# Optimization experiments

Measured on AMD Instinct MI355X. Metric: run time of the kernel, lower is better.

The kernel has to match this reference:

```python
import jax, jax.numpy as jnp
import numpy as np

N_NODES = 100000
N_EDGES = 1600000
B = 16
NMAX = 4096
IN_DIM = 32
H1 = 64      # capacity C
H2 = 128     # 2C
LAT = 64
DEC_H = 128  # 2C
DEC_IN = LAT + 2
FUEL = 5


def _ln(x, g, b):
    m = x.mean(-1, keepdims=True)
    v = x.var(-1, keepdims=True)
    return (x - m) / jnp.sqrt(v + 1e-5) * g + b


def _mlp2(x, wi, bi, g, be, wo, bo):
    # DeepMLP with num_layers=2: in_lin -> LayerNorm -> ReLU -> out_lin
    h = jax.nn.relu(_ln(x @ wi + bi, g, be))
    return h @ wo + bo


def setup_inputs() -> dict:
    key = jax.random.key(0)
    ks = jax.random.split(key, 48)
    d = {}
    d['x'] = jax.random.normal(ks[0], (N_NODES, IN_DIM), jnp.float32)
    d['edge_index'] = jax.random.randint(ks[1], (2, N_EDGES), 0, N_NODES)
    d['batch'] = jnp.sort(jax.random.randint(ks[2], (N_NODES,), 0, B))

    def w(k, shape):
        return (jax.random.normal(k, shape, jnp.float32) * 0.02)

    conv_shapes = {'w1m': (IN_DIM, H1), 'w2m': (H1, H2), 'w3m': (H2, LAT),
                   'w1l': (IN_DIM, H1), 'w2l': (H1, H2), 'w3l': (H2, LAT)}
    i = 3
    for nm, sh in conv_shapes.items():
        d[nm] = w(ks[i], sh); i += 1
        d['b' + nm[1:]] = jnp.zeros((sh[1],), jnp.float32)
    # node_mlp (DeepMLP dec_in->dec_h->dec_h)
    d['nm_wi'] = w(ks[i], (DEC_IN, DEC_H)); i += 1
    d['nm_bi'] = jnp.zeros((DEC_H,), jnp.float32)
    d['nm_g'] = jnp.ones((DEC_H,), jnp.float32)
    d['nm_be'] = jnp.zeros((DEC_H,), jnp.float32)
    d['nm_wo'] = w(ks[i], (DEC_H, DEC_H)); i += 1
    d['nm_bo'] = jnp.zeros((DEC_H,), jnp.float32)
    # heads
    d['ex_w'] = w(ks[i], (DEC_H, 1)); i += 1
    d['ex_b'] = jnp.zeros((1,), jnp.float32)
    d['fu_w'] = w(ks[i], (DEC_H, FUEL)); i += 1
    d['fu_b'] = jnp.zeros((FUEL,), jnp.float32)
    d['al_w'] = w(ks[i], (DEC_H, 1)); i += 1
    d['al_b'] = jnp.zeros((1,), jnp.float32)
    d['sl_w'] = w(ks[i], (DEC_H, 1)); i += 1
    d['sl_b'] = jnp.zeros((1,), jnp.float32)
    # edge_mlp (DeepMLP dec_in->dec_h->8)
    d['em_wi'] = w(ks[i], (DEC_IN, DEC_H)); i += 1
    d['em_bi'] = jnp.zeros((DEC_H,), jnp.float32)
    d['em_g'] = jnp.ones((DEC_H,), jnp.float32)
    d['em_be'] = jnp.zeros((DEC_H,), jnp.float32)
    d['em_wo'] = w(ks[i], (DEC_H, 8)); i += 1
    d['em_bo'] = jnp.zeros((8,), jnp.float32)
    d['pos_all'] = jax.random.normal(ks[i], (NMAX, 2), jnp.float32)
    return d


def reference(x, edge_index, batch,
              w1m, b1m, w2m, b2m, w3m, b3m,
              w1l, b1l, w2l, b2l, w3l, b3l,
              nm_wi, nm_bi, nm_g, nm_be, nm_wo, nm_bo,
              ex_w, ex_b, fu_w, fu_b, al_w, al_b, sl_w, sl_b,
              em_wi, em_bi, em_g, em_be, em_wo, em_bo,
              pos_all):
    # ---- GCN encoder with self-loops and symmetric normalization (PyG GCNConv) ----
    loops = jnp.arange(N_NODES)
    src = jnp.concatenate([edge_index[0], loops])
    dst = jnp.concatenate([edge_index[1], loops])
    deg = jax.ops.segment_sum(jnp.ones(src.shape, jnp.float32), dst, N_NODES)
    dinv = jax.lax.rsqrt(deg)  # deg >= 1 because of self-loops
    norm = (dinv[src] * dinv[dst])[:, None]

    def conv(h, wt, bt):
        hw = h @ wt                                   # [N, F_out]
        return jax.ops.segment_sum(norm * hw[src], dst, N_NODES) + bt

    mu = jax.nn.relu(conv(x, w1m, b1m))
    mu = jax.nn.relu(conv(mu, w2m, b2m))
    mu = jax.nn.relu(conv(mu, w3m, b3m))
    lg = jax.nn.relu(conv(x, w1l, b1l))
    lg = jax.nn.relu(conv(lg, w2l, b2l))
    lg = jax.nn.relu(conv(lg, w3l, b3l))

    cnt = jnp.maximum(jax.ops.segment_sum(jnp.ones((N_NODES,), jnp.float32), batch, B), 1.0)[:, None]
    mu_g = jax.ops.segment_sum(mu, batch, B) / cnt    # global_mean_pool [B, LAT]
    lg_g = jax.ops.segment_sum(lg, batch, B) / cnt

    z = mu_g  # eval-mode latent_sample returns mu

    # ---- decoder ----
    Z = jnp.broadcast_to(z[:, None, :], (B, NMAX, LAT))
    pos = jnp.broadcast_to(pos_all[None], (B, NMAX, 2))
    Zp = jnp.concatenate([Z, pos], -1).reshape(B * NMAX, DEC_IN)
    h = _mlp2(Zp, nm_wi, nm_bi, nm_g, nm_be, nm_wo, nm_bo)
    nodes = (h @ ex_w + ex_b).reshape(B, NMAX, 1)
    fuel = (h @ fu_w + fu_b).reshape(B, NMAX, FUEL)
    alt = (h @ al_w + al_b).reshape(B, NMAX, 1)
    slope = (h @ sl_w + sl_b).reshape(B, NMAX, 1)
    edges = _mlp2(Zp, em_wi, em_bi, em_g, em_be, em_wo, em_bo).reshape(B, NMAX, 8)
    return (nodes, edges, fuel, alt, slope, mu_g, lg_g)
```

## Files before the change

### kernel.cpp

```cpp
#include <hip/hip_runtime.h>
#include <hip/hip_bf16.h>

#define N_NODES 100000
#define N_EDGESC 1600000
#define BATCH_B 16
#define NMAXC 4096
#define LATC 64
#define NBINS 391
#define NSB 256
#define EPB ((N_EDGESC + NSB - 1) / NSB)
#define BIN_PAD 768

#define OUT_NODES 0
#define OUT_EDGES 65536
#define OUT_FUEL  589824
#define OUT_ALT   917504
#define OUT_SLOPE 983040
#define OUT_MU    1048576
#define OUT_LG    1049600

typedef float f32x2 __attribute__((ext_vector_type(2)));
typedef float f32x4 __attribute__((ext_vector_type(4)));
typedef short bf16x8 __attribute__((ext_vector_type(8)));
union U4B { uint4 u; bf16x8 b; };

__device__ __forceinline__ unsigned short f2bf(float f) {
    unsigned int u = __float_as_uint(f);
    return (unsigned short)((u + 0x7FFFu + ((u >> 16) & 1u)) >> 16);
}
__device__ __forceinline__ float bf2f(unsigned short h) {
    return __uint_as_float(((unsigned int)h) << 16);
}
__device__ __forceinline__ void f8acc(unsigned int u, float& a0, float& a1, float& a2, float& a3) {
    f32x2 lo = __builtin_amdgcn_cvt_pk_f32_fp8(u, false);
    f32x2 hi = __builtin_amdgcn_cvt_pk_f32_fp8(u, true);
    a0 += lo[0]; a1 += lo[1]; a2 += hi[0]; a3 += hi[1];
}

__global__ void batch_count(const int* __restrict__ batch, int* __restrict__ bcnt, int n) {
    int b = threadIdx.x;
    if (b >= BATCH_B) return;
    int lo = 0, hi = n;
    while (lo < hi) { int mid = (lo + hi) >> 1; if (batch[mid] < b) lo = mid + 1; else hi = mid; }
    int start = lo;
    lo = 0; hi = n;
    while (lo < hi) { int mid = (lo + hi) >> 1; if (batch[mid] <= b) lo = mid + 1; else hi = mid; }
    bcnt[b] = lo - start;
}

__global__ __launch_bounds__(1024) void histA(const int* __restrict__ dst, int* __restrict__ hist) {
    __shared__ int h[NBINS];
    int b = blockIdx.x, t = threadIdx.x;
    for (int i = t; i < NBINS; i += 1024) h[i] = 0;
    __syncthreads();
    int e0 = b * EPB, e1 = min(e0 + EPB, N_EDGESC);
    for (int i = e0 + t; i < e1; i += 1024)
        atomicAdd(&h[dst[i] >> 8], 1);
    __syncthreads();
    for (int i = t; i < NBINS; i += 1024) hist[i * NSB + b] = h[i];
}

__global__ void scanB(int* __restrict__ hist, int* __restrict__ total) {
    __shared__ int sh[NSB];
    int j = blockIdx.x, t = threadIdx.x;
    int v = hist[j * NSB + t];
    sh[t] = v; __syncthreads();
    for (int off = 1; off < NSB; off <<= 1) {
        int u = (t >= off) ? sh[t - off] : 0; __syncthreads();
        sh[t] += u; __syncthreads();
    }
    hist[j * NSB + t] = sh[t] - v;
    if (t == NSB - 1) total[j] = sh[t];
}

__global__ void scanC(const int* __restrict__ total, int* __restrict__ base) {
    __shared__ int sh[512];
    int t = threadIdx.x;
    int v = (t < NBINS) ? total[t] : 0;
    sh[t] = v; __syncthreads();
    for (int off = 1; off < 512; off <<= 1) {
        int u = (t >= off) ? sh[t - off] : 0; __syncthreads();
        sh[t] += u; __syncthreads();
    }
    if (t < NBINS) base[t] = sh[t] - v;
    if (t == NBINS - 1) base[NBINS] = sh[t];
}

__global__ __launch_bounds__(1024) void scatterD(const int* __restrict__ src, const int* __restrict__ dst,
                                                 const int* __restrict__ hist, const int* __restrict__ base,
                                                 unsigned int* __restrict__ sorted) {
    __shared__ int w0[NBINS];
    __shared__ int lc[NBINS];
    int b = blockIdx.x, t = threadIdx.x;
    for (int i = t; i < NBINS; i += 1024) {
        w0[i] = base[i] + hist[i * NSB + b];
        lc[i] = 0;
    }
    __syncthreads();
    int e0 = b * EPB, e1 = min(e0 + EPB, N_EDGESC);
    for (int i = e0 + t; i < e1; i += 1024) {
        int d = dst[i], s = src[i];
        int j = d >> 8;
        int r = atomicAdd(&lc[j], 1);
        sorted[w0[j] + r] = ((unsigned int)s << 8) | (d & 255);
    }
}

__global__ void csr_compact(const unsigned int* __restrict__ sorted, const int* __restrict__ base,
                            int* __restrict__ adj, int* __restrict__ offs,
                            int* __restrict__ cnt, float* __restrict__ dinv, int N) {
    __shared__ int lc[256];
    __shared__ int cur[256];
    __shared__ int so4[256];
    int j = blockIdx.x, t = threadIdx.x;
    lc[t] = 0; cur[t] = 0;
    __syncthreads();
    int e0 = base[j], e1 = base[j + 1];
    for (int i = e0 + t; i < e1; i += 256)
        atomicAdd(&lc[sorted[i] & 255], 1);
    __syncthreads();
    int c4 = (lc[t] + 3) & ~3;
    so4[t] = c4;
    __syncthreads();
    for (int off = 1; off < 256; off <<= 1) {
        int u = (t >= off) ? so4[t - off] : 0; __syncthreads();
        so4[t] += u; __syncthreads();
    }
    int mybase = base[j] + j * BIN_PAD + so4[t] - c4;
    __syncthreads();
    so4[t] = mybase;
    __syncthreads();
    for (int i = e0 + t; i < e1; i += 256) {
        unsigned int pk = sorted[i];
        int d = pk & 255;
        int r = atomicAdd(&cur[d], 1);
        adj[so4[d] + r] = (int)(pk >> 8);
    }
    int n = j * 256 + t;
    if (n < N) {
        cnt[n] = lc[t];
        offs[n] = so4[t];
        dinv[n] = rsqrtf((float)(lc[t] + 1));
    }
}

__global__ void prescale_x(const float* __restrict__ x, const float* __restrict__ dinv,
                           unsigned int* __restrict__ xs8, int total4) {
    int i4 = blockIdx.x * 256 + threadIdx.x;
    if (i4 < total4) {
        float4 v = *(const float4*)&x[i4 * 4];
        float ds = dinv[i4 >> 3] * 64.f;
        unsigned int r = 0;
        r = __builtin_amdgcn_cvt_pk_fp8_f32(v.x * ds, v.y * ds, r, false);
        r = __builtin_amdgcn_cvt_pk_fp8_f32(v.z * ds, v.w * ds, r, true);
        xs8[i4] = r;
    }
}

__global__ void agg_s32(const unsigned int* __restrict__ xs8, const int* __restrict__ cnt,
                        const int* __restrict__ offs, const int* __restrict__ adj,
                        const float* __restrict__ dinv, float* __restrict__ out, int N) {
    int t = threadIdx.x;
    int sub = t >> 3, f = t & 7;
    int n = blockIdx.x * 32 + sub;
    if (n >= N) return;
    float s0 = 0.f, s1 = 0.f, s2 = 0.f, s3 = 0.f;
    f8acc(xs8[(size_t)n * 8 + f], s0, s1, s2, s3);
    int e = offs[n];
    int e1 = e + cnt[n];
    for (; e + 8 <= e1; e += 8) {
        int4 ia = *(const int4*)&adj[e];
        int4 ib = *(const int4*)&adj[e + 4];
        unsigned int u0 = xs8[(size_t)ia.x * 8 + f];
        unsigned int u1 = xs8[(size_t)ia.y * 8 + f];
        unsigned int u2 = xs8[(size_t)ia.z * 8 + f];
        unsigned int u3 = xs8[(size_t)ia.w * 8 + f];
        unsigned int u4 = xs8[(size_t)ib.x * 8 + f];
        unsigned int u5 = xs8[(size_t)ib.y * 8 + f];
        unsigned int u6 = xs8[(size_t)ib.z * 8 + f];
        unsigned int u7 = xs8[(size_t)ib.w * 8 + f];
        f8acc(u0, s0, s1, s2, s3); f8acc(u1, s0, s1, s2, s3);
        f8acc(u2, s0, s1, s2, s3); f8acc(u3, s0, s1, s2, s3);
        f8acc(u4, s0, s1, s2, s3); f8acc(u5, s0, s1, s2, s3);
        f8acc(u6, s0, s1, s2, s3); f8acc(u7, s0, s1, s2, s3);
    }
    if (e + 4 <= e1) {
        int4 ia = *(const int4*)&adj[e];
        unsigned int u0 = xs8[(size_t)ia.x * 8 + f];
// ... 38 lines not shown
        f8acc(u4, s0, s1, s2, s3); f8acc(u5, s0, s1, s2, s3);
        f8acc(u6, s0, s1, s2, s3); f8acc(u7, s0, s1, s2, s3);
    }
    if (e + 4 <= e1) {
        int4 ia = *(const int4*)&adj[e];
        unsigned int u0 = tbl[(size_t)ia.x * 32 + f];
        unsigned int u1 = tbl[(size_t)ia.y * 32 + f];
        unsigned int u2 = tbl[(size_t)ia.z * 32 + f];
        unsigned int u3 = tbl[(size_t)ia.w * 32 + f];
        f8acc(u0, s0, s1, s2, s3); f8acc(u1, s0, s1, s2, s3);
        f8acc(u2, s0, s1, s2, s3); f8acc(u3, s0, s1, s2, s3);
        e += 4;
    }
    for (; e < e1; e++) f8acc(tbl[(size_t)adj[e] * 32 + f], s0, s1, s2, s3);
    float d = dinv[n] * (1.f / 32.f);
    float v0 = s0 * d, v1 = s1 * d, v2 = s2 * d, v3 = s3 * d;
    if (BIASRELU) {
        float4 bv = *(const float4*)&bias[4 * f];
        v0 = fmaxf(v0 + bv.x, 0.f); v1 = fmaxf(v1 + bv.y, 0.f);
        v2 = fmaxf(v2 + bv.z, 0.f); v3 = fmaxf(v3 + bv.w, 0.f);
    }
    if (OUT8) {
        unsigned int r = 0;
        r = __builtin_amdgcn_cvt_pk_fp8_f32(v0 * 32.f, v1 * 32.f, r, false);
        r = __builtin_amdgcn_cvt_pk_fp8_f32(v2 * 32.f, v3 * 32.f, r, true);
        ((unsigned int*)outv)[(size_t)n * 32 + f] = r;
    } else {
        ushort4 u;
        u.x = f2bf(v0); u.y = f2bf(v1); u.z = f2bf(v2); u.w = f2bf(v3);
        *(ushort4*)&((unsigned short*)outv)[(size_t)n * 128 + 4 * f] = u;
    }
}

template <int K, int F>
__global__ void wprep(const float* __restrict__ Wa, const float* __restrict__ Wb,
                      unsigned int* __restrict__ wfrag) {
    constexpr int S = K / 32, C = F / 16;
    int lane = threadIdx.x;
    int bc = blockIdx.x;
    int c = bc % C;
    int s = (bc / C) % S;
    int y = bc / (C * S);
    const float* W = (y == 0) ? Wa : Wb;
    int col = c * 16 + (lane & 15);
    int k0 = s * 32 + (lane >> 4) * 8;
    unsigned int q[4];
#pragma unroll
    for (int jj = 0; jj < 4; jj++) {
        float lo = W[(size_t)(k0 + 2 * jj) * F + col];
        float hi = W[(size_t)(k0 + 2 * jj + 1) * F + col];
        q[jj] = (unsigned int)f2bf(lo) | ((unsigned int)f2bf(hi) << 16);
    }
    *(uint4*)&wfrag[((size_t)bc * 64 + lane) * 4] = make_uint4(q[0], q[1], q[2], q[3]);
}

template <int K, int F, int IN_STRIDE, int IN_OFF_Y, int OUT_STRIDE, int OUT_OFF_Y,
          bool BIASRELU, bool SCALE, int INMODE, int OUTMODE>
__global__ __launch_bounds__(256) void mfma_conv(
    const void* __restrict__ inv, const unsigned int* __restrict__ wfrag,
    const float* __restrict__ biasa, const float* __restrict__ biasb,
    const float* __restrict__ dinv, void* __restrict__ outv, int N) {
    constexpr int S = K / 32, C = F / 16;
    constexpr int FP = F + 4;
    __shared__ unsigned short buf[4][16][FP];
    int t = threadIdx.x, lane = t & 63, wave = t >> 6;
    int y = blockIdx.y;
    int n0 = blockIdx.x * 64 + wave * 16;
    const float* bias = (y == 0) ? biasa : biasb;
    const unsigned int* wf = wfrag + (size_t)y * S * C * 64 * 4;

    f32x4 acc[C];
#pragma unroll
    for (int c = 0; c < C; c++) acc[c] = (f32x4)(0.f);

    int arow = n0 + (lane & 15);
    bool aok = arow < N;
#pragma unroll
    for (int s = 0; s < S; s++) {
        U4B af; af.u = make_uint4(0u, 0u, 0u, 0u);
        if (aok) {
            if constexpr (INMODE == 2) {
                uint2 u = *(const uint2*)((const unsigned char*)inv +
                            (size_t)arow * IN_STRIDE + y * IN_OFF_Y + s * 32 + (lane >> 4) * 8);
                f32x2 p0 = __builtin_amdgcn_cvt_pk_f32_fp8(u.x, false);
                f32x2 p1 = __builtin_amdgcn_cvt_pk_f32_fp8(u.x, true);
                f32x2 p2 = __builtin_amdgcn_cvt_pk_f32_fp8(u.y, false);
                f32x2 p3 = __builtin_amdgcn_cvt_pk_f32_fp8(u.y, true);
                af.u.x = (unsigned int)f2bf(p0[0]) | ((unsigned int)f2bf(p0[1]) << 16);
                af.u.y = (unsigned int)f2bf(p1[0]) | ((unsigned int)f2bf(p1[1]) << 16);
                af.u.z = (unsigned int)f2bf(p2[0]) | ((unsigned int)f2bf(p2[1]) << 16);
                af.u.w = (unsigned int)f2bf(p3[0]) | ((unsigned int)f2bf(p3[1]) << 16);
            } else if constexpr (INMODE == 1) {
                af.u = *(const uint4*)((const unsigned short*)inv +
                            (size_t)arow * IN_STRIDE + y * IN_OFF_Y + s * 32 + (lane >> 4) * 8);
            } else {
                const float* ap = (const float*)inv + (size_t)arow * IN_STRIDE + y * IN_OFF_Y
                                  + s * 32 + (lane >> 4) * 8;
                float4 v0 = *(const float4*)ap;
                float4 v1 = *(const float4*)(ap + 4);
                af.u.x = (unsigned int)f2bf(v0.x) | ((unsigned int)f2bf(v0.y) << 16);
                af.u.y = (unsigned int)f2bf(v0.z) | ((unsigned int)f2bf(v0.w) << 16);
                af.u.z = (unsigned int)f2bf(v1.x) | ((unsigned int)f2bf(v1.y) << 16);
                af.u.w = (unsigned int)f2bf(v1.z) | ((unsigned int)f2bf(v1.w) << 16);
            }
        }
#pragma unroll
        for (int c = 0; c < C; c++) {
            U4B wb;
            wb.u = *(const uint4*)&wf[((size_t)(s * C + c) * 64 + lane) * 4];
            acc[c] = __builtin_amdgcn_mfma_f32_16x16x32_bf16(af.b, wb.b, acc[c], 0, 0, 0);
        }
    }

    constexpr float ISC = (INMODE == 2) ? (1.f / 32.f) : 1.f;
#pragma unroll
    for (int c = 0; c < C; c++) {
        int col = c * 16 + (lane & 15);
        float bv = BIASRELU ? bias[col] : 0.f;
#pragma unroll
        for (int r = 0; r < 4; r++) {
            int row = (lane >> 4) * 4 + r;
            int n = n0 + row;
            float v = acc[c][r] * ISC;
            if (BIASRELU) v = fmaxf(v + bv, 0.f);
            if (SCALE) v *= dinv[min(n, N - 1)];
            buf[wave][row][col] = f2bf(v);
        }
    }
    __syncthreads();

    constexpr int CPR = F / 8;
    for (int i = t; i < 64 * CPR; i += 256) {
        int row = i / CPR;
        int f0 = (i % CPR) * 8;
        int n = blockIdx.x * 64 + row;
        if (n >= N) continue;
        const unsigned short* bp = &buf[row >> 4][row & 15][f0];
        uint2 a = *(const uint2*)bp;
        uint2 b = *(const uint2*)(bp + 4);
        size_t off = (size_t)n * OUT_STRIDE + y * OUT_OFF_Y + f0;
        if constexpr (OUTMODE == 2) {
            float e0 = __uint_as_float(a.x << 16), e1 = __uint_as_float(a.x & 0xFFFF0000u);
            float e2 = __uint_as_float(a.y << 16), e3 = __uint_as_float(a.y & 0xFFFF0000u);
            float e4 = __uint_as_float(b.x << 16), e5 = __uint_as_float(b.x & 0xFFFF0000u);
            float e6 = __uint_as_float(b.y << 16), e7 = __uint_as_float(b.y & 0xFFFF0000u);
            unsigned int r0 = 0, r1 = 0;
            r0 = __builtin_amdgcn_cvt_pk_fp8_f32(e0 * 32.f, e1 * 32.f, r0, false);
            r0 = __builtin_amdgcn_cvt_pk_fp8_f32(e2 * 32.f, e3 * 32.f, r0, true);
            r1 = __builtin_amdgcn_cvt_pk_fp8_f32(e4 * 32.f, e5 * 32.f, r1, false);
            r1 = __builtin_amdgcn_cvt_pk_fp8_f32(e6 * 32.f, e7 * 32.f, r1, true);
            *(uint2*)((unsigned char*)outv + off) = make_uint2(r0, r1);
        } else {
            *(uint4*)((unsigned short*)outv + off) = make_uint4(a.x, a.y, b.x, b.y);
        }
    }
}

__global__ void prep_cat(const float* __restrict__ w1m, const float* __restrict__ w1l,
                         const float* __restrict__ b1m, const float* __restrict__ b1l,
                         const float* __restrict__ b3m, const float* __restrict__ b3l,
                         float* __restrict__ wcat1, float* __restrict__ bcat1,
                         float* __restrict__ bcat3) {
    int i = blockIdx.x * 256 + threadIdx.x;
    if (i < 32 * 128) {
        int k = i >> 7, f = i & 127;
        wcat1[i] = (f < 64) ? w1m[k * 64 + f] : w1l[k * 64 + f - 64];
    } else if (i < 32 * 128 + 128) {
        int f = i - 32 * 128;
        bcat1[f] = (f < 64) ? b1m[f] : b1l[f - 64];
    } else if (i < 32 * 128 + 256) {
        int f = i - 32 * 128 - 128;
        bcat3[f] = (f < 64) ? b3m[f] : b3l[f - 64];
    }
}

__global__ void prep_dec(const float* __restrict__ nm_wo, const float* __restrict__ nm_bo,
                         const float* __restrict__ ex_w, const float* __restrict__ ex_b,
                         const float* __restrict__ fu_w, const float* __restrict__ fu_b,
                         const float* __restrict__ al_w, const float* __restrict__ al_b,
                         const float* __restrict__ sl_w, const float* __restrict__ sl_b,
                         const float* __restrict__ em_wo,
                         float* __restrict__ wtn, float* __restrict__ bcn,
                         float* __restrict__ wte) {
    int idx = blockIdx.x * 256 + threadIdx.x;
    if (idx < 1024) {
        int j = idx >> 7, k = idx & 127;
        float s = 0.f;
        for (int m = 0; m < 128; m++) {
            float w = (j == 0) ? ex_w[m] : (j <= 5) ? fu_w[m * 5 + (j - 1)]
                     : (j == 6) ? al_w[m] : sl_w[m];
            s += nm_wo[k * 128 + m] * w;
        }
        wtn[j * 128 + k] = s;
    } else if (idx < 2048) {
        int i2 = idx - 1024;
        int j = i2 >> 7, k = i2 & 127;
        wte[j * 128 + k] = em_wo[k * 8 + j];
    } else if (idx < 2056) {
        int j = idx - 2048;
        float s = (j == 0) ? ex_b[0] : (j <= 5) ? fu_b[j - 1] : (j == 6) ? al_b[0] : sl_b[0];
        for (int m = 0; m < 128; m++) {
            float w = (j == 0) ? ex_w[m] : (j <= 5) ? fu_w[m * 5 + (j - 1)]
                     : (j == 6) ? al_w[m] : sl_w[m];
            s += nm_bo[m] * w;
        }
        bcn[j] = s;
    }
}

#define POOL_CHUNK 128
__global__ void pool128(const unsigned int* __restrict__ h, const int* __restrict__ batch,
                        float* __restrict__ sums, int n) {
    int f = threadIdx.x;
    int s0 = blockIdx.x * POOL_CHUNK;
    if (s0 >= n) return;
    int s1 = min(s0 + POOL_CHUNK, n);
    int cur = batch[s0];
    float a0 = 0.f, a1 = 0.f;
    for (int i = s0; i < s1; i++) {
        int b = batch[i];
        if (b != cur) {
            atomicAdd(&sums[cur * 128 + 2 * f], a0);
            atomicAdd(&sums[cur * 128 + 2 * f + 1], a1);
            a0 = a1 = 0.f; cur = b;
        }
        unsigned int u = h[(size_t)i * 64 + f];
        a0 += __uint_as_float(u << 16);
        a1 += __uint_as_float(u & 0xFFFF0000u);
    }
    atomicAdd(&sums[cur * 128 + 2 * f], a0);
    atomicAdd(&sums[cur * 128 + 2 * f + 1], a1);
}

__global__ void finalize_pool(const float* __restrict__ sums, const int* __restrict__ bcnt,
                              float* __restrict__ out, float* __restrict__ zbuf) {
    int i = blockIdx.x * 1024 + threadIdx.x;
    int b = i >> 7, f = i & 127;
    float c = fmaxf((float)bcnt[b], 1.f);
    float v = sums[i] / c;
    if (f < 64) { out[OUT_MU + b * 64 + f] = v; zbuf[b * 64 + f] = v; }
    else out[OUT_LG + b * 64 + (f - 64)] = v;
}

__global__ void zwi_kernel(const float* __restrict__ z,
                           const float* __restrict__ nm_wi, const float* __restrict__ nm_bi,
                           const float* __restrict__ em_wi, const float* __restrict__ em_bi,
                           float* __restrict__ zwi_nm, float* __restrict__ zwi_em) {
    int b = blockIdx.x, t = threadIdx.x;
    float an = nm_bi[t], ae = em_bi[t];
    for (int k = 0; k < 64; k++) {
        float zv = z[b * 64 + k];
        an += zv * nm_wi[k * 128 + t];
        ae += zv * em_wi[k * 128 + t];
    }
    zwi_nm[b * 128 + t] = an;
    zwi_em[b * 128 + t] = ae;
}

#define D3_ROWS 32

__global__ __launch_bounds__(256) void decoder3(
    const float* __restrict__ zwi_nm, const float* __restrict__ zwi_em,
    const float* __restrict__ nm_wi, const float* __restrict__ em_wi,
    const float* __restrict__ nm_g, const float* __restrict__ nm_be,
    const float* __restrict__ em_g, const float* __restrict__ em_be,
    const float* __restrict__ wtn, const float* __restrict__ bcn,
    const float* __restrict__ wte, const float* __restrict__ em_bo,
    const float* __restrict__ pos_all,
    float* __restrict__ out) {
    __shared__ float sn[D3_ROWS][132];
    __shared__ float se[D3_ROWS][132];
    __shared__ float Wn[8][132];
    __shared__ float We[8][132];
    int t = threadIdx.x;
    int lane = t & 63, wave = t >> 6;
    int rowBase = blockIdx.x * D3_ROWS;
    int b = rowBase >> 12;
    int row0 = rowBase + wave * 8;

    for (int i = t; i < 1024; i += 256) {
        Wn[i >> 7][i & 127] = wtn[i];
        We[i >> 7][i & 127] = wte[i];
    }

// ... 62 lines not shown
    const float* x    = (const float*)d_in[0];
    const int* edge   = (const int*)d_in[1];
    const int* batch  = (const int*)d_in[2];
    const float* w1m = (const float*)d_in[3];  const float* b1m = (const float*)d_in[4];
    const float* w2m = (const float*)d_in[5];  const float* b2m = (const float*)d_in[6];
    const float* w3m = (const float*)d_in[7];  const float* b3m = (const float*)d_in[8];
    const float* w1l = (const float*)d_in[9];  const float* b1l = (const float*)d_in[10];
    const float* w2l = (const float*)d_in[11]; const float* b2l = (const float*)d_in[12];
    const float* w3l = (const float*)d_in[13]; const float* b3l = (const float*)d_in[14];
    const float* nm_wi = (const float*)d_in[15]; const float* nm_bi = (const float*)d_in[16];
    const float* nm_g  = (const float*)d_in[17]; const float* nm_be = (const float*)d_in[18];
    const float* nm_wo = (const float*)d_in[19]; const float* nm_bo = (const float*)d_in[20];
    const float* ex_w = (const float*)d_in[21]; const float* ex_b = (const float*)d_in[22];
    const float* fu_w = (const float*)d_in[23]; const float* fu_b = (const float*)d_in[24];
    const float* al_w = (const float*)d_in[25]; const float* al_b = (const float*)d_in[26];
    const float* sl_w = (const float*)d_in[27]; const float* sl_b = (const float*)d_in[28];
    const float* em_wi = (const float*)d_in[29]; const float* em_bi = (const float*)d_in[30];
    const float* em_g  = (const float*)d_in[31]; const float* em_be = (const float*)d_in[32];
    const float* em_wo = (const float*)d_in[33]; const float* em_bo = (const float*)d_in[34];
    const float* pos_all = (const float*)d_in[35];
    float* out = (float*)d_out;

    char* p = (char*)d_ws;
    auto alloc = [&](size_t bytes) -> void* {
        void* r = (void*)p;
        p += ((bytes + 255) / 256) * 256;
        return r;
    };
    int* cnt      = (int*)alloc((size_t)N_NODES * 4);
    int* offs     = (int*)alloc((size_t)N_NODES * 4);
    float* dinv   = (float*)alloc((size_t)N_NODES * 4);
    int* bcnt     = (int*)alloc(BATCH_B * 4);
    float* sums   = (float*)alloc(BATCH_B * 128 * 4);
    float* zbuf   = (float*)alloc(BATCH_B * LATC * 4);
    float* zwi_nm = (float*)alloc(BATCH_B * 128 * 4);
    float* zwi_em = (float*)alloc(BATCH_B * 128 * 4);
    float* wcat1  = (float*)alloc(32 * 128 * 4);
    float* bcat1  = (float*)alloc(128 * 4);
    float* bcat3  = (float*)alloc(128 * 4);
    float* wtn    = (float*)alloc(8 * 128 * 4);
    float* bcn    = (float*)alloc(8 * 4);
    float* wte    = (float*)alloc(8 * 128 * 4);
    unsigned int* wf1 = (unsigned int*)alloc((size_t)1 * 1 * 8 * 64 * 4 * 4);
    unsigned int* wf2 = (unsigned int*)alloc((size_t)2 * 2 * 8 * 64 * 4 * 4);
    unsigned int* wf3 = (unsigned int*)alloc((size_t)2 * 4 * 4 * 64 * 4 * 4);
    int* hist     = (int*)alloc((size_t)NBINS * NSB * 4);
    int* total    = (int*)alloc((size_t)NBINS * 4);
    int* base     = (int*)alloc((size_t)(NBINS + 1) * 4);
    unsigned int* sorted = (unsigned int*)alloc((size_t)N_EDGESC * 4);
    int* adj      = (int*)alloc((size_t)(N_EDGESC + NBINS * BIN_PAD + 256) * 4);
    unsigned int* xs8 = (unsigned int*)alloc((size_t)N_NODES * 8 * 4);
    float* agg0   = (float*)alloc((size_t)N_NODES * 32 * 4);
    unsigned int* hA8 = (unsigned int*)alloc((size_t)N_NODES * 32 * 4);
    unsigned int* hB8 = (unsigned int*)alloc((size_t)N_NODES * 32 * 4);
    unsigned short* h256 = (unsigned short*)alloc((size_t)N_NODES * 256 * 2);
    unsigned short* final128 = (unsigned short*)alloc((size_t)N_NODES * 128 * 2);
    unsigned int* hD8 = hA8;

    const int* srcp = edge;
    const int* dstp = edge + N_EDGESC;

    hipMemsetAsync(sums, 0, (size_t)BATCH_B * 128 * 4, stream);

    histA<<<NSB, 1024, 0, stream>>>(dstp, hist);
    scanB<<<NBINS, NSB, 0, stream>>>(hist, total);
    scanC<<<1, 512, 0, stream>>>(total, base);
    scatterD<<<NSB, 1024, 0, stream>>>(srcp, dstp, hist, base, sorted);
    csr_compact<<<NBINS, 256, 0, stream>>>(sorted, base, adj, offs, cnt, dinv, N_NODES);

    batch_count<<<1, 64, 0, stream>>>(batch, bcnt, N_NODES);
    prep_cat<<<17, 256, 0, stream>>>(w1m, w1l, b1m, b1l, b3m, b3l, wcat1, bcat1, bcat3);
    prep_dec<<<9, 256, 0, stream>>>(nm_wo, nm_bo, ex_w, ex_b, fu_w, fu_b, al_w, al_b,
                                    sl_w, sl_b, em_wo, wtn, bcn, wte);
    wprep<32, 128><<<1 * 1 * 8, 64, 0, stream>>>(wcat1, wcat1, wf1);
    wprep<64, 128><<<2 * 2 * 8, 64, 0, stream>>>(w2m, w2l, wf2);
    wprep<128, 64><<<2 * 4 * 4, 64, 0, stream>>>(w3m, w3l, wf3);
    prescale_x<<<(N_NODES * 8 + 255) / 256, 256, 0, stream>>>(x, dinv, xs8, N_NODES * 8);

    agg_s32<<<(N_NODES + 31) / 32, 256, 0, stream>>>(xs8, cnt, offs, adj, dinv, agg0, N_NODES);

    const int GB = (N_NODES + 63) / 64;

    mfma_conv<32, 128, 32, 0, 128, 0, true, true, 0, 2>
        <<<dim3(GB, 1), 256, 0, stream>>>(agg0, wf1, bcat1, bcat1, dinv, hA8, N_NODES);

    agg128<false, true><<<(N_NODES + 7) / 8, 256, 0, stream>>>(
        hA8, cnt, offs, adj, dinv, nullptr, hB8, N_NODES);

    mfma_conv<64, 128, 128, 64, 256, 128, true, false, 2, 1>
        <<<dim3(GB, 2), 256, 0, stream>>>(hB8, wf2, b2m, b2l, dinv, h256, N_NODES);

    mfma_conv<128, 64, 256, 128, 128, 64, false, true, 1, 2>
        <<<dim3(GB, 2), 256, 0, stream>>>(h256, wf3, nullptr, nullptr, dinv, hD8, N_NODES);

    agg128<true, false><<<(N_NODES + 7) / 8, 256, 0, stream>>>(
        hD8, cnt, offs, adj, dinv, bcat3, final128, N_NODES);

    pool128<<<(N_NODES + POOL_CHUNK - 1) / POOL_CHUNK, 64, 0, stream>>>(
        (const unsigned int*)final128, batch, sums, N_NODES);
    finalize_pool<<<2, 1024, 0, stream>>>(sums, bcnt, out, zbuf);

    zwi_kernel<<<BATCH_B, 128, 0, stream>>>(zbuf, nm_wi, nm_bi, em_wi, em_bi, zwi_nm, zwi_em);

    decoder3<<<BATCH_B * NMAXC / D3_ROWS, 256, 0, stream>>>(
        zwi_nm, zwi_em, nm_wi, em_wi, nm_g, nm_be, em_g, em_be,
        wtn, bcn, wte, em_bo, pos_all, out);
}
```

Baseline: 297.2 us.

## Fuse prep kernels, fold x prescale into CSR compaction, fuse conv layers 2 and 3

Merges batch counting, bias concatenation, decoder weight folding and all MFMA weight-fragment preparation into one mega_prep launch. Folds the fp8 prescale of x into csr_compact, fuses the layer-2 and layer-3 dense transforms into one conv23 kernel that keeps the 128-wide hidden tile in shared memory instead of writing h256 to global, and merges pool finalization with the z·W_in kernel. The aim is to cut launch count and the round trip of the 100k x 256 bf16 intermediate, in exchange for more shared memory and register use per block in the fused conv.

Result: faster. 265.9 us (-10.5%).

```diff
diff --git a/kernel.cpp b/kernel.cpp
--- a/kernel.cpp
+++ b/kernel.cpp
@@ -36,16 +36,11 @@
     f32x2 hi = __builtin_amdgcn_cvt_pk_f32_fp8(u, true);
     a0 += lo[0]; a1 += lo[1]; a2 += hi[0]; a3 += hi[1];
 }
-
-__global__ void batch_count(const int* __restrict__ batch, int* __restrict__ bcnt, int n) {
-    int b = threadIdx.x;
-    if (b >= BATCH_B) return;
-    int lo = 0, hi = n;
-    while (lo < hi) { int mid = (lo + hi) >> 1; if (batch[mid] < b) lo = mid + 1; else hi = mid; }
-    int start = lo;
-    lo = 0; hi = n;
-    while (lo < hi) { int mid = (lo + hi) >> 1; if (batch[mid] <= b) lo = mid + 1; else hi = mid; }
-    bcnt[b] = lo - start;
+__device__ __forceinline__ void f8_to_bf2(unsigned int u, unsigned int& q0, unsigned int& q1) {
+    f32x2 lo = __builtin_amdgcn_cvt_pk_f32_fp8(u, false);
+    f32x2 hi = __builtin_amdgcn_cvt_pk_f32_fp8(u, true);
+    q0 = (unsigned int)f2bf(lo[0]) | ((unsigned int)f2bf(lo[1]) << 16);
+    q1 = (unsigned int)f2bf(hi[0]) | ((unsigned int)f2bf(hi[1]) << 16);
 }
 
 __global__ __launch_bounds__(1024) void histA(const int* __restrict__ dst, int* __restrict__ hist) {
@@ -107,8 +102,10 @@
 }
 
 __global__ void csr_compact(const unsigned int* __restrict__ sorted, const int* __restrict__ base,
+                            const float* __restrict__ x,
                             int* __restrict__ adj, int* __restrict__ offs,
-                            int* __restrict__ cnt, float* __restrict__ dinv, int N) {
+                            int* __restrict__ cnt, float* __restrict__ dinv,
+                            unsigned int* __restrict__ xs8, int N) {
     __shared__ int lc[256];
     __shared__ int cur[256];
     __shared__ int so4[256];
@@ -138,22 +135,24 @@
     }
     int n = j * 256 + t;
     if (n < N) {
-        cnt[n] = lc[t];
+        int c = lc[t];
+        cnt[n] = c;
         offs[n] = so4[t];
-        dinv[n] = rsqrtf((float)(lc[t] + 1));
-    }
-}
-
-__global__ void prescale_x(const float* __restrict__ x, const float* __restrict__ dinv,
-                           unsigned int* __restrict__ xs8, int total4) {
-    int i4 = blockIdx.x * 256 + threadIdx.x;
-    if (i4 < total4) {
-        float4 v = *(const float4*)&x[i4 * 4];
-        float ds = dinv[i4 >> 3] * 64.f;
-        unsigned int r = 0;
-        r = __builtin_amdgcn_cvt_pk_fp8_f32(v.x * ds, v.y * ds, r, false);
-        r = __builtin_amdgcn_cvt_pk_fp8_f32(v.z * ds, v.w * ds, r, true);
-        xs8[i4] = r;
+        float dv = rsqrtf((float)(c + 1));
+        dinv[n] = dv;
+        float ds = dv * 64.f;
+        const float* xr = &x[(size_t)n * 32];
+        unsigned int q[8];
+#pragma unroll
+        for (int jj = 0; jj < 8; jj++) {
+            float4 v = *(const float4*)&xr[jj * 4];
+            unsigned int r8 = 0;
+            r8 = __builtin_amdgcn_cvt_pk_fp8_f32(v.x * ds, v.y * ds, r8, false);
+            r8 = __builtin_amdgcn_cvt_pk_fp8_f32(v.z * ds, v.w * ds, r8, true);
+            q[jj] = r8;
+        }
+        *(uint4*)&xs8[(size_t)n * 8] = make_uint4(q[0], q[1], q[2], q[3]);
+        *(uint4*)&xs8[(size_t)n * 8 + 4] = make_uint4(q[4], q[5], q[6], q[7]);
     }
 }
 
@@ -258,18 +257,8 @@
     }
 }
 
-template <int K, int F>
-__global__ void wprep(const float* __restrict__ Wa, const float* __restrict__ Wb,
-                      unsigned int* __restrict__ wfrag) {
-    constexpr int S = K / 32, C = F / 16;
-    int lane = threadIdx.x;
-    int bc = blockIdx.x;
-    int c = bc % C;
-    int s = (bc / C) % S;
-    int y = bc / (C * S);
-    const float* W = (y == 0) ? Wa : Wb;
-    int col = c * 16 + (lane & 15);
-    int k0 = s * 32 + (lane >> 4) * 8;
+__device__ __forceinline__ void wfrag_write(const float* W, int F, int col, int k0,
+                                            unsigned int* dst) {
     unsigned int q[4];
 #pragma unroll
     for (int jj = 0; jj < 4; jj++) {
@@ -277,23 +266,107 @@
         float hi = W[(size_t)(k0 + 2 * jj + 1) * F + col];
         q[jj] = (unsigned int)f2bf(lo) | ((unsigned int)f2bf(hi) << 16);
     }
-    *(uint4*)&wfrag[((size_t)bc * 64 + lane) * 4] = make_uint4(q[0], q[1], q[2], q[3]);
-}
-
-template <int K, int F, int IN_STRIDE, int IN_OFF_Y, int OUT_STRIDE, int OUT_OFF_Y,
-          bool BIASRELU, bool SCALE, int INMODE, int OUTMODE>
-__global__ __launch_bounds__(256) void mfma_conv(
-    const void* __restrict__ inv, const unsigned int* __restrict__ wfrag,
-    const float* __restrict__ biasa, const float* __restrict__ biasb,
-    const float* __restrict__ dinv, void* __restrict__ outv, int N) {
-    constexpr int S = K / 32, C = F / 16;
-    constexpr int FP = F + 4;
+    *(uint4*)dst = make_uint4(q[0], q[1], q[2], q[3]);
+}
+
+__global__ void mega_prep(const int* __restrict__ batch,
+                          const float* __restrict__ w1m, const float* __restrict__ w1l,
+                          const float* __restrict__ b1m, const float* __restrict__ b1l,
+                          const float* __restrict__ b3m, const float* __restrict__ b3l,
+                          const float* __restrict__ w2m, const float* __restrict__ w2l,
+                          const float* __restrict__ w3m, const float* __restrict__ w3l,
+                          const float* __restrict__ nm_wo, const float* __restrict__ nm_bo,
+                          const float* __restrict__ ex_w, const float* __restrict__ ex_b,
+                          const float* __restrict__ fu_w, const float* __restrict__ fu_b,
+                          const float* __restrict__ al_w, const float* __restrict__ al_b,
+                          const float* __restrict__ sl_w, const float* __restrict__ sl_b,
+                          const float* __restrict__ em_wo,
+                          int* __restrict__ bcnt, float* __restrict__ bcat1,
+                          float* __restrict__ bcat3, float* __restrict__ wtn,
+                          float* __restrict__ bcn, float* __restrict__ wte,
+                          unsigned int* __restrict__ wf1, unsigned int* __restrict__ wf2,
+                          unsigned int* __restrict__ wf3) {
+    int blk = blockIdx.x, t = threadIdx.x;
+    if (blk == 0) {
+        if (t < 128) bcat1[t] = (t < 64) ? b1m[t] : b1l[t - 64];
+        else { int f = t - 128; bcat3[f] = (f < 64) ? b3m[f] : b3l[f - 64]; }
+        if (t < BATCH_B) {
+            int b = t;
+            int lo = 0, hi = N_NODES;
+            while (lo < hi) { int mid = (lo + hi) >> 1; if (batch[mid] < b) lo = mid + 1; else hi = mid; }
+            int start = lo;
+            lo = 0; hi = N_NODES;
+            while (lo < hi) { int mid = (lo + hi) >> 1; if (batch[mid] <= b) lo = mid + 1; else hi = mid; }
+            bcnt[b] = lo - start;
+        }
+    } else if (blk <= 9) {
+        int idx = (blk - 1) * 256 + t;
+        if (idx < 1024) {
+            int j = idx >> 7, k = idx & 127;
+            float s = 0.f;
+            for (int m = 0; m < 128; m++) {
+                float w = (j == 0) ? ex_w[m] : (j <= 5) ? fu_w[m * 5 + (j - 1)]
+                         : (j == 6) ? al_w[m] : sl_w[m];
+                s += nm_wo[k * 128 + m] * w;
+            }
+            wtn[j * 128 + k] = s;
+        } else if (idx < 2048) {
+            int i2 = idx - 1024;
+            int j = i2 >> 7, k = i2 & 127;
+            wte[j * 128 + k] = em_wo[k * 8 + j];
+        } else if (idx < 2056) {
+            int j = idx - 2048;
+            float s = (j == 0) ? ex_b[0] : (j <= 5) ? fu_b[j - 1] : (j == 6) ? al_b[0] : sl_b[0];
+            for (int m = 0; m < 128; m++) {
+                float w = (j == 0) ? ex_w[m] : (j <= 5) ? fu_w[m * 5 + (j - 1)]
+                         : (j == 6) ? al_w[m] : sl_w[m];
+                s += nm_bo[m] * w;
+            }
+            bcn[j] = s;
+        }
+    } else if (blk <= 17) {
+        if (t < 64) {
+            int c = blk - 10;
+            int col = c * 16 + (t & 15);
+            int k0 = (t >> 4) * 8;
+            unsigned int q[4];
+#pragma unroll
+            for (int jj = 0; jj < 4; jj++) {
+                int ka = k0 + 2 * jj, kb = ka + 1;
+                float lo = (col < 64) ? w1m[ka * 64 + col] : w1l[ka * 64 + col - 64];
+                float hi = (col < 64) ? w1m[kb * 64 + col] : w1l[kb * 64 + col - 64];
+                q[jj] = (unsigned int)f2bf(lo) | ((unsigned int)f2bf(hi) << 16);
+            }
+            *(uint4*)&wf1[((size_t)c * 64 + t) * 4] = make_uint4(q[0], q[1], q[2], q[3]);
+        }
+    } else if (blk <= 49) {
+        if (t < 64) {
+            int bc = blk - 18;
+            int c = bc % 8, s = (bc / 8) % 2, y = bc / 16;
+            const float* W = y ? w2l : w2m;
+            wfrag_write(W, 128, c * 16 + (t & 15), s * 32 + (t >> 4) * 8,
+                        &wf2[((size_t)bc * 64 + t) * 4]);
+        }
+    } else {
+        if (t < 64) {
+            int bc = blk - 50;
+            int c = bc % 4, s = (bc / 4) % 4, y = bc / 16;
+            const float* W = y ? w3l : w3m;
+            wfrag_write(W, 64, c * 16 + (t & 15), s * 32 + (t >> 4) * 8,
+                        &wf3[((size_t)bc * 64 + t) * 4]);
+        }
+    }
+}
+
+__global__ __launch_bounds__(256) void mfma_conv1(
+    const float* __restrict__ inv, const unsigned int* __restrict__ wfrag,
+    const float* __restrict__ bias, const float* __restrict__ dinv,
+    unsigned int* __restrict__ outv, int N) {
+    constexpr int C = 8;
+    constexpr int FP = 132;
     __shared__ unsigned short buf[4][16][FP];
     int t = threadIdx.x, lane = t & 63, wave = t >> 6;
-    int y = blockIdx.y;
     int n0 = blockIdx.x * 64 + wave * 16;
-    const float* bias = (y == 0) ? biasa : biasb;
-    const unsigned int* wf = wfrag + (size_t)y * S * C * 64 * 4;
 
     f32x4 acc[C];
 #pragma unroll
@@ -301,136 +374,149 @@
 
     int arow = n0 + (lane & 15);
     bool aok = arow < N;
-#pragma unroll
-    for (int s = 0; s < S; s++) {
-        U4B af; af.u = make_uint4(0u, 0u, 0u, 0u);
-        if (aok) {
-            if constexpr (INMODE == 2) {
-                uint2 u = *(const uint2*)((const unsigned char*)inv +
-                            (size_t)arow * IN_STRIDE + y * IN_OFF_Y + s * 32 + (lane >> 4) * 8);
-                f32x2 p0 = __builtin_amdgcn_cvt_pk_f32_fp8(u.x, false);
-                f32x2 p1 = __builtin_amdgcn_cvt_pk_f32_fp8(u.x, true);
-                f32x2 p2 = __builtin_amdgcn_cvt_pk_f32_fp8(u.y, false);
-                f32x2 p3 = __builtin_amdgcn_cvt_pk_f32_fp8(u.y, true);
-                af.u.x = (unsigned int)f2bf(p0[0]) | ((unsigned int)f2bf(p0[1]) << 16);
-                af.u.y = (unsigned int)f2bf(p1[0]) | ((unsigned int)f2bf(p1[1]) << 16);
-                af.u.z = (unsigned int)f2bf(p2[0]) | ((unsigned int)f2bf(p2[1]) << 16);
-                af.u.w = (unsigned int)f2bf(p3[0]) | ((unsigned int)f2bf(p3[1]) << 16);
-            } else if constexpr (INMODE == 1) {
-                af.u = *(const uint4*)((const unsigned short*)inv +
-                            (size_t)arow * IN_STRIDE + y * IN_OFF_Y + s * 32 + (lane >> 4) * 8);
-            } else {
-                const float* ap = (const float*)inv + (size_t)arow * IN_STRIDE + y * IN_OFF_Y
-                                  + s * 32 + (lane >> 4) * 8;
-                float4 v0 = *(const float4*)ap;
-                float4 v1 = *(const float4*)(ap + 4);
-                af.u.x = (unsigned int)f2bf(v0.x) | ((unsigned int)f2bf(v0.y) << 16);
-                af.u.y = (unsigned int)f2bf(v0.z) | ((unsigned int)f2bf(v0.w) << 16);
-                af.u.z = (unsigned int)f2bf(v1.x) | ((unsigned int)f2bf(v1.y) << 16);
-                af.u.w = (unsigned int)f2bf(v1.z) | ((unsigned int)f2bf(v1.w) << 16);
-            }
-        }
-#pragma unroll
-        for (int c = 0; c < C; c++) {
-            U4B wb;
-            wb.u = *(const uint4*)&wf[((size_t)(s * C + c) * 64 + lane) * 4];
-            acc[c] = __builtin_amdgcn_mfma_f32_16x16x32_bf16(af.b, wb.b, acc[c], 0, 0, 0);
-        }
-    }
-
-    constexpr float ISC = (INMODE == 2) ? (1.f / 32.f) : 1.f;
+    U4B af; af.u = make_uint4(0u, 0u, 0u, 0u);
+    if (aok) {
+        const float* ap = inv + (size_t)arow * 32 + (lane >> 4) * 8;
+        float4 v0 = *(const float4*)ap;
+        float4 v1 = *(const float4*)(ap + 4);
+        af.u.x = (unsigned int)f2bf(v0.x) | ((unsigned int)f2bf(v0.y) << 16);
+        af.u.y = (unsigned int)f2bf(v0.z) | ((unsigned int)f2bf(v0.w) << 16);
+        af.u.z = (unsigned int)f2bf(v1.x) | ((unsigned int)f2bf(v1.y) << 16);
+        af.u.w = (unsigned int)f2bf(v1.z) | ((unsigned int)f2bf(v1.w) << 16);
+    }
+#pragma unroll
+    for (int c = 0; c < C; c++) {
+        U4B wb;
+        wb.u = *(const uint4*)&wfrag[((size_t)c * 64 + lane) * 4];
+        acc[c] = __builtin_amdgcn_mfma_f32_16x16x32_bf16(af.b, wb.b, acc[c], 0, 0, 0);
+    }
+
 #pragma unroll
     for (int c = 0; c < C; c++) {
         int col = c * 16 + (lane & 15);
-        float bv = BIASRELU ? bias[col] : 0.f;
+        float bv = bias[col];
 #pragma unroll
         for (int r = 0; r < 4; r++) {
             int row = (lane >> 4) * 4 + r;
             int n = n0 + row;
-            float v = acc[c][r] * ISC;
-            if (BIASRELU) v = fmaxf(v + bv, 0.f);
-            if (SCALE) v *= dinv[min(n, N - 1)];
+            float v = fmaxf(acc[c][r] + bv, 0.f) * dinv[min(n, N - 1)];
             buf[wave][row][col] = f2bf(v);
         }
     }
     __syncthreads();
 
-    constexpr int CPR = F / 8;
-    for (int i = t; i < 64 * CPR; i += 256) {
-        int row = i / CPR;
-        int f0 = (i % CPR) * 8;
+    for (int i = t; i < 64 * 16; i += 256) {
+        int row = i / 16;
+        int f0 = (i % 16) * 8;
         int n = blockIdx.x * 64 + row;
         if (n >= N) continue;
         const unsigned short* bp = &buf[row >> 4][row & 15][f0];
         uint2 a = *(const uint2*)bp;
         uint2 b = *(const uint2*)(bp + 4);
-        size_t off = (size_t)n * OUT_STRIDE + y * OUT_OFF_Y + f0;
-        if constexpr (OUTMODE == 2) {
-            float e0 = __uint_as_float(a.x << 16), e1 = __uint_as_float(a.x & 0xFFFF0000u);
-            float e2 = __uint_as_float(a.y << 16), e3 = __uint_as_float(a.y & 0xFFFF0000u);
-            float e4 = __uint_as_float(b.x << 16), e5 = __uint_as_float(b.x & 0xFFFF0000u);
-            float e6 = __uint_as_float(b.y << 16), e7 = __uint_as_float(b.y & 0xFFFF0000u);
-            unsigned int r0 = 0, r1 = 0;
-            r0 = __builtin_amdgcn_cvt_pk_fp8_f32(e0 * 32.f, e1 * 32.f, r0, false);
-            r0 = __builtin_amdgcn_cvt_pk_fp8_f32(e2 * 32.f, e3 * 32.f, r0, true);
-            r1 = __builtin_amdgcn_cvt_pk_fp8_f32(e4 * 32.f, e5 * 32.f, r1, false);
-            r1 = __builtin_amdgcn_cvt_pk_fp8_f32(e6 * 32.f, e7 * 32.f, r1, true);
-            *(uint2*)((unsigned char*)outv + off) = make_uint2(r0, r1);
-        } else {
-            *(uint4*)((unsigned short*)outv + off) = make_uint4(a.x, a.y, b.x, b.y);
-        }
-    }
-}
-
-__global__ void prep_cat(const float* __restrict__ w1m, const float* __restrict__ w1l,
-                         const float* __restrict__ b1m, const float* __restrict__ b1l,
-                         const float* __restrict__ b3m, const float* __restrict__ b3l,
-                         float* __restrict__ wcat1, float* __restrict__ bcat1,
-                         float* __restrict__ bcat3) {
-    int i = blockIdx.x * 256 + threadIdx.x;
-    if (i < 32 * 128) {
-        int k = i >> 7, f = i & 127;
-        wcat1[i] = (f < 64) ? w1m[k * 64 + f] : w1l[k * 64 + f - 64];
-    } else if (i < 32 * 128 + 128) {
-        int f = i - 32 * 128;
-        bcat1[f] = (f < 64) ? b1m[f] : b1l[f - 64];
-    } else if (i < 32 * 128 + 256) {
-        int f = i - 32 * 128 - 128;
-        bcat3[f] = (f < 64) ? b3m[f] : b3l[f - 64];
-    }
-}
-
-__global__ void prep_dec(const float* __restrict__ nm_wo, const float* __restrict__ nm_bo,
-                         const float* __restrict__ ex_w, const float* __restrict__ ex_b,
-                         const float* __restrict__ fu_w, const float* __restrict__ fu_b,
-                         const float* __restrict__ al_w, const float* __restrict__ al_b,
-                         const float* __restrict__ sl_w, const float* __restrict__ sl_b,
-                         const float* __restrict__ em_wo,
-                         float* __restrict__ wtn, float* __restrict__ bcn,
-                         float* __restrict__ wte) {
-    int idx = blockIdx.x * 256 + threadIdx.x;
-    if (idx < 1024) {
-        int j = idx >> 7, k = idx & 127;
-        float s = 0.f;
-        for (int m = 0; m < 128; m++) {
-            float w = (j == 0) ? ex_w[m] : (j <= 5) ? fu_w[m * 5 + (j - 1)]
-                     : (j == 6) ? al_w[m] : sl_w[m];
-            s += nm_wo[k * 128 + m] * w;
-        }
-        wtn[j * 128 + k] = s;
-    } else if (idx < 2048) {
-        int i2 = idx - 1024;
-        int j = i2 >> 7, k = i2 & 127;
-        wte[j * 128 + k] = em_wo[k * 8 + j];
-    } else if (idx < 2056) {
-        int j = idx - 2048;
-        float s = (j == 0) ? ex_b[0] : (j <= 5) ? fu_b[j - 1] : (j == 6) ? al_b[0] : sl_b[0];
-        for (int m = 0; m < 128; m++) {
-            float w = (j == 0) ? ex_w[m] : (j <= 5) ? fu_w[m * 5 + (j - 1)]
-                     : (j == 6) ? al_w[m] : sl_w[m];
-            s += nm_bo[m] * w;
-        }
-        bcn[j] = s;
+        float e0 = __uint_as_float(a.x << 16), e1 = __uint_as_float(a.x & 0xFFFF0000u);
+        float e2 = __uint_as_float(a.y << 16), e3 = __uint_as_float(a.y & 0xFFFF0000u);
+        float e4 = __uint_as_float(b.x << 16), e5 = __uint_as_float(b.x & 0xFFFF0000u);
+        float e6 = __uint_as_float(b.y << 16), e7 = __uint_as_float(b.y & 0xFFFF0000u);
+        unsigned int r0 = 0, r1 = 0;
+        r0 = __builtin_amdgcn_cvt_pk_fp8_f32(e0 * 32.f, e1 * 32.f, r0, false);
+        r0 = __builtin_amdgcn_cvt_pk_fp8_f32(e2 * 32.f, e3 * 32.f, r0, true);
+        r1 = __builtin_amdgcn_cvt_pk_fp8_f32(e4 * 32.f, e5 * 32.f, r1, false);
+        r1 = __builtin_amdgcn_cvt_pk_fp8_f32(e6 * 32.f, e7 * 32.f, r1, true);
+        *(uint2*)((unsigned char*)outv + (size_t)n * 128 + f0) = make_uint2(r0, r1);
+    }
+}
+
+__global__ __launch_bounds__(256) void conv23(
+    const unsigned int* __restrict__ hB8, const unsigned int* __restrict__ wf2,
+    const unsigned int* __restrict__ wf3, const float* __restrict__ b2m,
+    const float* __restrict__ b2l, const float* __restrict__ dinv,
+    unsigned int* __restrict__ hD8, int N) {
+    __shared__ unsigned short hbuf[4][16][136];
+    __shared__ unsigned short obuf[4][16][72];
+    int t = threadIdx.x, lane = t & 63, wave = t >> 6;
+    int y = blockIdx.y;
+    int n0 = blockIdx.x * 64 + wave * 16;
+    const float* bias = y ? b2l : b2m;
+    const unsigned int* w2 = wf2 + (size_t)y * 2 * 8 * 64 * 4;
+    const unsigned int* w3 = wf3 + (size_t)y * 4 * 4 * 64 * 4;
+
+    f32x4 acc2[8];
+#pragma unroll
+    for (int c = 0; c < 8; c++) acc2[c] = (f32x4)(0.f);
+    int arow = n0 + (lane & 15);
+    bool aok = arow < N;
+#pragma unroll
+    for (int s = 0; s < 2; s++) {
+        U4B af; af.u = make_uint4(0u, 0u, 0u, 0u);
+        if (aok) {
+            uint2 u = *(const uint2*)((const unsigned char*)hB8 +
+                        (size_t)arow * 128 + y * 64 + s * 32 + (lane >> 4) * 8);
+            f8_to_bf2(u.x, af.u.x, af.u.y);
+            f8_to_bf2(u.y, af.u.z, af.u.w);
+        }
+#pragma unroll
+        for (int c = 0; c < 8; c++) {
+            U4B wb;
+            wb.u = *(const uint4*)&w2[((size_t)(s * 8 + c) * 64 + lane) * 4];
+            acc2[c] = __builtin_amdgcn_mfma_f32_16x16x32_bf16(af.b, wb.b, acc2[c], 0, 0, 0);
+        }
+    }
+#pragma unroll
+    for (int c = 0; c < 8; c++) {
+        int col = c * 16 + (lane & 15);
+        float bv = bias[col];
+#pragma unroll
+        for (int r = 0; r < 4; r++) {
+            int row = (lane >> 4) * 4 + r;
+            float v = fmaxf(acc2[c][r] * (1.f / 32.f) + bv, 0.f);
+            hbuf[wave][row][col] = f2bf(v);
+        }
+    }
+
+    f32x4 acc3[4];
+#pragma unroll
+    for (int c = 0; c < 4; c++) acc3[c] = (f32x4)(0.f);
+#pragma unroll
+    for (int s = 0; s < 4; s++) {
+        U4B af;
+        af.u = *(const uint4*)&hbuf[wave][lane & 15][s * 32 + (lane >> 4) * 8];
+#pragma unroll
+        for (int c = 0; c < 4; c++) {
+            U4B wb;
+            wb.u = *(const uint4*)&w3[((size_t)(s * 4 + c) * 64 + lane) * 4];
+            acc3[c] = __builtin_amdgcn_mfma_f32_16x16x32_bf16(af.b, wb.b, acc3[c], 0, 0, 0);
+        }
+    }
+#pragma unroll
+    for (int c = 0; c < 4; c++) {
+        int col = c * 16 + (lane & 15);
+#pragma unroll
+        for (int r = 0; r < 4; r++) {
+            int row = (lane >> 4) * 4 + r;
+            int n = n0 + row;
+            float v = acc3[c][r] * dinv[min(n, N - 1)];
+            obuf[wave][row][col] = f2bf(v);
+        }
+    }
+    __syncthreads();
+    for (int i = t; i < 64 * 8; i += 256) {
+        int row = i / 8;
+        int f0 = (i % 8) * 8;
+        int n = blockIdx.x * 64 + row;
+        if (n >= N) continue;
+        const unsigned short* bp = &obuf[row >> 4][row & 15][f0];
+        uint2 a = *(const uint2*)bp;
+        uint2 b = *(const uint2*)(bp + 4);
+        float e0 = __uint_as_float(a.x << 16), e1 = __uint_as_float(a.x & 0xFFFF0000u);
+        float e2 = __uint_as_float(a.y << 16), e3 = __uint_as_float(a.y & 0xFFFF0000u);
+        float e4 = __uint_as_float(b.x << 16), e5 = __uint_as_float(b.x & 0xFFFF0000u);
+        float e6 = __uint_as_float(b.y << 16), e7 = __uint_as_float(b.y & 0xFFFF0000u);
+        unsigned int r0 = 0, r1 = 0;
+        r0 = __builtin_amdgcn_cvt_pk_fp8_f32(e0 * 32.f, e1 * 32.f, r0, false);
+        r0 = __builtin_amdgcn_cvt_pk_fp8_f32(e2 * 32.f, e3 * 32.f, r0, true);
+        r1 = __builtin_amdgcn_cvt_pk_fp8_f32(e4 * 32.f, e5 * 32.f, r1, false);
+        r1 = __builtin_amdgcn_cvt_pk_fp8_f32(e6 * 32.f, e7 * 32.f, r1, true);
+        *(uint2*)((unsigned char*)hD8 + (size_t)n * 128 + y * 64 + f0) = make_uint2(r0, r1);
     }
 }
 
@@ -458,24 +544,21 @@
     atomicAdd(&sums[cur * 128 + 2 * f + 1], a1);
 }
 
-__global__ void finalize_pool(const float* __restrict__ sums, const int* __restrict__ bcnt,
-                              float* __restrict__ out, float* __restrict__ zbuf) {
-    int i = blockIdx.x * 1024 + threadIdx.x;
-    int b = i >> 7, f = i & 127;
+__global__ void finalize_zwi(const float* __restrict__ sums, const int* __restrict__ bcnt,
+                             const float* __restrict__ nm_wi, const float* __restrict__ nm_bi,
+                             const float* __restrict__ em_wi, const float* __restrict__ em_bi,
+                             float* __restrict__ out, float* __restrict__ zwi_nm,
+                             float* __restrict__ zwi_em) {
+    __shared__ float zs[64];
+    int b = blockIdx.x, t = threadIdx.x;
     float c = fmaxf((float)bcnt[b], 1.f);
-    float v = sums[i] / c;
-    if (f < 64) { out[OUT_MU + b * 64 + f] = v; zbuf[b * 64 + f] = v; }
-    else out[OUT_LG + b * 64 + (f - 64)] = v;
-}
-
-__global__ void zwi_kernel(const float* __restrict__ z,
-                           const float* __restrict__ nm_wi, const float* __restrict__ nm_bi,
-                           const float* __restrict__ em_wi, const float* __restrict__ em_bi,
-                           float* __restrict__ zwi_nm, float* __restrict__ zwi_em) {
-    int b = blockIdx.x, t = threadIdx.x;
+    float v = sums[b * 128 + t] / c;
+    if (t < 64) { out[OUT_MU + b * 64 + t] = v; zs[t] = v; }
+    else out[OUT_LG + b * 64 + (t - 64)] = v;
+    __syncthreads();
     float an = nm_bi[t], ae = em_bi[t];
     for (int k = 0; k < 64; k++) {
-        float zv = z[b * 64 + k];
+        float zv = zs[k];
         an += zv * nm_wi[k * 128 + t];
         ae += zv * em_wi[k * 128 + t];
     }
@@ -604,18 +687,16 @@
     float* dinv   = (float*)alloc((size_t)N_NODES * 4);
     int* bcnt     = (int*)alloc(BATCH_B * 4);
     float* sums   = (float*)alloc(BATCH_B * 128 * 4);
-    float* zbuf   = (float*)alloc(BATCH_B * LATC * 4);
     float* zwi_nm = (float*)alloc(BATCH_B * 128 * 4);
     float* zwi_em = (float*)alloc(BATCH_B * 128 * 4);
-    float* wcat1  = (float*)alloc(32 * 128 * 4);
     float* bcat1  = (float*)alloc(128 * 4);
     float* bcat3  = (float*)alloc(128 * 4);
     float* wtn    = (float*)alloc(8 * 128 * 4);
     float* bcn    = (float*)alloc(8 * 4);
     float* wte    = (float*)alloc(8 * 128 * 4);
-    unsigned int* wf1 = (unsigned int*)alloc((size_t)1 * 1 * 8 * 64 * 4 * 4);
-    unsigned int* wf2 = (unsigned int*)alloc((size_t)2 * 2 * 8 * 64 * 4 * 4);
-    unsigned int* wf3 = (unsigned int*)alloc((size_t)2 * 4 * 4 * 64 * 4 * 4);
+    unsigned int* wf1 = (unsigned int*)alloc((size_t)8 * 64 * 4 * 4);
+    unsigned int* wf2 = (unsigned int*)alloc((size_t)32 * 64 * 4 * 4);
+    unsigned int* wf3 = (unsigned int*)alloc((size_t)32 * 64 * 4 * 4);
     int* hist     = (int*)alloc((size_t)NBINS * NSB * 4);
     int* total    = (int*)alloc((size_t)NBINS * 4);
     int* base     = (int*)alloc((size_t)(NBINS + 1) * 4);
@@ -625,7 +706,6 @@
     float* agg0   = (float*)alloc((size_t)N_NODES * 32 * 4);
     unsigned int* hA8 = (unsigned int*)alloc((size_t)N_NODES * 32 * 4);
     unsigned int* hB8 = (unsigned int*)alloc((size_t)N_NODES * 32 * 4);
-    unsigned short* h256 = (unsigned short*)alloc((size_t)N_NODES * 256 * 2);
     unsigned short* final128 = (unsigned short*)alloc((size_t)N_NODES * 128 * 2);
     unsigned int* hD8 = hA8;
 
@@ -633,46 +713,37 @@
     const int* dstp = edge + N_EDGESC;
 
     hipMemsetAsync(sums, 0, (size_t)BATCH_B * 128 * 4, stream);
+
+    mega_prep<<<82, 256, 0, stream>>>(batch, w1m, w1l, b1m, b1l, b3m, b3l,
+                                      w2m, w2l, w3m, w3l, nm_wo, nm_bo,
+                                      ex_w, ex_b, fu_w, fu_b, al_w, al_b, sl_w, sl_b,
+                                      em_wo, bcnt, bcat1, bcat3, wtn, bcn, wte,
+                                      wf1, wf2, wf3);
 
     histA<<<NSB, 1024, 0, stream>>>(dstp, hist);
     scanB<<<NBINS, NSB, 0, stream>>>(hist, total);
     scanC<<<1, 512, 0, stream>>>(total, base);
     scatterD<<<NSB, 1024, 0, stream>>>(srcp, dstp, hist, base, sorted);
-    csr_compact<<<NBINS, 256, 0, stream>>>(sorted, base, adj, offs, cnt, dinv, N_NODES);
-
-    batch_count<<<1, 64, 0, stream>>>(batch, bcnt, N_NODES);
-    prep_cat<<<17, 256, 0, stream>>>(w1m, w1l, b1m, b1l, b3m, b3l, wcat1, bcat1, bcat3);
-    prep_dec<<<9, 256, 0, stream>>>(nm_wo, nm_bo, ex_w, ex_b, fu_w, fu_b, al_w, al_b,
-                                    sl_w, sl_b, em_wo, wtn, bcn, wte);
-    wprep<32, 128><<<1 * 1 * 8, 64, 0, stream>>>(wcat1, wcat1, wf1);
-    wprep<64, 128><<<2 * 2 * 8, 64, 0, stream>>>(w2m, w2l, wf2);
-    wprep<128, 64><<<2 * 4 * 4, 64, 0, stream>>>(w3m, w3l, wf3);
-    prescale_x<<<(N_NODES * 8 + 255) / 256, 256, 0, stream>>>(x, dinv, xs8, N_NODES * 8);
+    csr_compact<<<NBINS, 256, 0, stream>>>(sorted, base, x, adj, offs, cnt, dinv, xs8, N_NODES);
 
     agg_s32<<<(N_NODES + 31) / 32, 256, 0, stream>>>(xs8, cnt, offs, adj, dinv, agg0, N_NODES);
 
     const int GB = (N_NODES + 63) / 64;
 
-    mfma_conv<32, 128, 32, 0, 128, 0, true, true, 0, 2>
-        <<<dim3(GB, 1), 256, 0, stream>>>(agg0, wf1, bcat1, bcat1, dinv, hA8, N_NODES);
+    mfma_conv1<<<GB, 256, 0, stream>>>(agg0, wf1, bcat1, dinv, hA8, N_NODES);
 
     agg128<false, true><<<(N_NODES + 7) / 8, 256, 0, stream>>>(
         hA8, cnt, offs, adj, dinv, nullptr, hB8, N_NODES);
 
-    mfma_conv<64, 128, 128, 64, 256, 128, true, false, 2, 1>
-        <<<dim3(GB, 2), 256, 0, stream>>>(hB8, wf2, b2m, b2l, dinv, h256, N_NODES);
-
-    mfma_conv<128, 64, 256, 128, 128, 64, false, true, 1, 2>
-        <<<dim3(GB, 2), 256, 0, stream>>>(h256, wf3, nullptr, nullptr, dinv, hD8, N_NODES);
+    conv23<<<dim3(GB, 2), 256, 0, stream>>>(hB8, wf2, wf3, b2m, b2l, dinv, hD8, N_NODES);
 
     agg128<true, false><<<(N_NODES + 7) / 8, 256, 0, stream>>>(
         hD8, cnt, offs, adj, dinv, bcat3, final128, N_NODES);
 
     pool128<<<(N_NODES + POOL_CHUNK - 1) / POOL_CHUNK, 64, 0, stream>>>(
         (const unsigned int*)final128, batch, sums, N_NODES);
-    finalize_pool<<<2, 1024, 0, stream>>>(sums, bcnt, out, zbuf);
-
-    zwi_kernel<<<BATCH_B, 128, 0, stream>>>(zbuf, nm_wi, nm_bi, em_wi, em_bi, zwi_nm, zwi_em);
+    finalize_zwi<<<BATCH_B, 128, 0, stream>>>(sums, bcnt, nm_wi, nm_bi, em_wi, em_bi,
+                                              out, zwi_nm, zwi_em);
 
     decoder3<<<BATCH_B * NMAXC / D3_ROWS, 256, 0, stream>>>(
         zwi_nm, zwi_em, nm_wi, em_wi, nm_g, nm_be, em_g, em_be,
```
